# Performance work log

Measured on AMD Instinct MI355X. Metric: run time of the kernel, lower is better.

The kernel has to match this reference:

```python
import jax, jax.numpy as jnp
import numpy as np
import math

B, S, E = 2, 2048, 1024
H = 16
D = E // H  # head dim = 64


def setup_inputs() -> dict:
    key = jax.random.key(0)
    ks = jax.random.split(key, 9)
    s = 1.0 / math.sqrt(E)
    return {
        "x": jax.random.normal(ks[0], (B, S, E), dtype=jnp.float32),
        "Wq": jax.random.uniform(ks[1], (E, E), jnp.float32, -s, s),
        "bq": jnp.zeros((E,), jnp.float32),
        "Wk": jax.random.uniform(ks[2], (E, E), jnp.float32, -s, s),
        "bk": jnp.zeros((E,), jnp.float32),
        "Wv": jax.random.uniform(ks[3], (E, E), jnp.float32, -s, s),
        "bv": jnp.zeros((E,), jnp.float32),
        "Wo": jax.random.uniform(ks[4], (E, E), jnp.float32, -s, s),
        "bo": jnp.zeros((E,), jnp.float32),
    }


def reference(x, Wq, bq, Wk, bk, Wv, bv, Wo, bo):
    b, s, e = x.shape
    q = x @ Wq + bq  # [B,S,E]
    k = x @ Wk + bk
    v = x @ Wv + bv
    # [B,S,E] -> [B,H,S,D]
    q = q.reshape(b, s, H, D).transpose(0, 2, 1, 3)
    k = k.reshape(b, s, H, D).transpose(0, 2, 1, 3)
    v = v.reshape(b, s, H, D).transpose(0, 2, 1, 3)
    scores = jnp.einsum('bhqd,bhkd->bhqk', q, k) / jnp.sqrt(jnp.float32(D))
    causal = jnp.tril(jnp.ones((s, s), dtype=bool))  # keep lower triangle
    scores = jnp.where(causal, scores, -jnp.inf)
    attn = jax.nn.softmax(scores, axis=-1)
    # dropout is identity in eval mode
    out = jnp.einsum('bhqk,bhkd->bhqd', attn, v)
    out = out.transpose(0, 2, 1, 3).reshape(b, s, e)
    return out @ Wo + bo
```

## Files before the change

kernel.cpp:

```cpp
#include <hip/hip_runtime.h>
#include <hip/hip_bf16.h>
#include <math.h>

#define B_ 2
#define S_ 2048
#define E_ 1024
#define H_ 16
#define D_ 64
#define M_ (B_*S_)

typedef __attribute__((ext_vector_type(8))) short short8v;
typedef __attribute__((ext_vector_type(4))) float floatx4;

__device__ __forceinline__ short f2bf(float f) {
    union { float f; unsigned u; } x; x.f = f;
    unsigned r = (x.u + 0x7fffu + ((x.u >> 16) & 1u)) >> 16;
    return (short)r;
}

__device__ __forceinline__ unsigned pk_bf16(float a, float b) {
    union { float f; unsigned u; } x, y;
    x.f = a; y.f = b;
    return __builtin_amdgcn_perm(y.u + 0x8000u, x.u + 0x8000u, 0x07060302u);
}

__device__ __forceinline__ float fast_exp2(float x) {
#if __has_builtin(__builtin_amdgcn_exp2f)
    return __builtin_amdgcn_exp2f(x);
#else
    return __expf(x * 0.6931471805599453f);
#endif
}

__device__ __forceinline__ void gl2lds16(const void* g, void* l) {
    __builtin_amdgcn_global_load_lds(
        (const __attribute__((address_space(1))) void*)g,
        (__attribute__((address_space(3))) void*)l, 16, 0, 0);
}

__device__ __forceinline__ int swz_off(int row, int cg) {
    return row*64 + (((cg ^ (row & 7)) & 7) << 3);
}

__global__ __launch_bounds__(256) void prep(
    const float* __restrict__ x, short* __restrict__ xb,
    const float* __restrict__ W0, const float* __restrict__ W1,
    const float* __restrict__ W2, const float* __restrict__ W3,
    short* __restrict__ T0, short* __restrict__ T1,
    short* __restrict__ T2, short* __restrict__ T3)
{
    const int bid = blockIdx.x;
    if (bid < 2048) {
        const size_t i = ((size_t)bid*256 + threadIdx.x) * 8;
        float4 a = *(const float4*)(x + i);
        float4 b = *(const float4*)(x + i + 4);
        int4 p = { (int)pk_bf16(a.x,a.y), (int)pk_bf16(a.z,a.w),
                   (int)pk_bf16(b.x,b.y), (int)pk_bf16(b.z,b.w) };
        *(int4*)(xb + i) = p;
        return;
    }
    const int tb = bid - 2048;
    const int z = tb >> 10;
    const float* W = (z==0)?W0:(z==1)?W1:(z==2)?W2:W3;
    short*       T = (z==0)?T0:(z==1)?T1:(z==2)?T2:T3;
    __shared__ float tile[32][33];
    const int k0 = ((tb>>5)&31)*32, n0 = (tb&31)*32;
    const int r = threadIdx.x >> 5, c = threadIdx.x & 31;
    #pragma unroll
    for (int i=0;i<4;i++)
        tile[r+8*i][c] = W[(size_t)(k0+r+8*i)*E_ + n0 + c];
    __syncthreads();
    #pragma unroll
    for (int i=0;i<4;i++)
        T[(size_t)(n0+r+8*i)*E_ + k0 + c] = f2bf(tile[c][r+8*i]);
}

__global__ __launch_bounds__(512, 2) void qkv_gemm(
    const short* __restrict__ xb, const short* __restrict__ Wt,
    const float* __restrict__ bq, const float* __restrict__ bk, const float* __restrict__ bv,
    short* __restrict__ Qo, short* __restrict__ Ko, short* __restrict__ Vo)
{
    __shared__ __align__(16) short As[2][256*64];
    __shared__ __align__(16) short Bs[2][192*64];

    const int t = threadIdx.x;
    const int wave = t >> 6, lane = t & 63;
    const int quad = lane >> 4, l15 = lane & 15;
    const int wr = wave >> 2, wc = wave & 3;

    const int bid = blockIdx.x;
    const int sw  = (bid & 7) * 32 + (bid >> 3);
    const int m0  = (sw >> 4) * 256;
    const int nf0 = (sw & 15) * 192;

    const int sr8 = lane >> 3;
    const int scs = ((lane & 7) ^ sr8) * 8;

    const short* Ag = xb + (size_t)m0  * E_;
    const short* Bg = Wt + (size_t)nf0 * E_;

    floatx4 acc[8][3];
    #pragma unroll
    for (int i=0;i<8;i++)
        #pragma unroll
        for (int j=0;j<3;j++) acc[i][j] = (floatx4){0.f,0.f,0.f,0.f};

    auto stageA = [&](int p, int h, int kt) {
        const int rb = h*128 + wave*16;
        const short* src = Ag + (size_t)(rb + sr8)*E_ + kt*64 + scs;
        #pragma unroll
        for (int c=0;c<2;c++)
            gl2lds16(src + (size_t)c*8*E_, &As[p][(rb + c*8)*64]);
    };
    auto stageB = [&](int p, int u, int kt) {
        const int rb = u*64 + wave*8;
        gl2lds16(Bg + (size_t)(rb + sr8)*E_ + kt*64 + scs, &Bs[p][rb*64]);
    };

    short8v a[2][2], b[3][2];
    auto rdA = [&](int p, int row16, int ks) -> short8v {
        return *(const short8v*)&As[p][swz_off(wr*128 + row16*16 + l15, quad + ks*4)];
    };
    auto rdB = [&](int p, int row16, int ks) -> short8v {
        return *(const short8v*)&Bs[p][swz_off(wc*48 + row16*16 + l15, quad + ks*4)];
    };
    auto lda2 = [&](int p, int mbase) {
        #pragma unroll
        for (int j=0;j<2;j++)
            #pragma unroll
            for (int ks=0;ks<2;ks++) a[j][ks] = rdA(p, mbase+j, ks);
    };
    auto mm = [&](int mbase) {
        #pragma unroll
        for (int j=0;j<2;j++)
            #pragma unroll
            for (int nt=0;nt<3;nt++)
                #pragma unroll
                for (int ks=0;ks<2;ks++)
                    acc[mbase+j][nt] = __builtin_amdgcn_mfma_f32_16x16x32_bf16(
                        a[j][ks], b[nt][ks], acc[mbase+j][nt], 0,0,0);
    };

    auto ktile = [&](int tt, int p) {
        #pragma unroll
        for (int nt=0;nt<3;nt++)
            #pragma unroll
            for (int ks=0;ks<2;ks++) b[nt][ks] = rdB(p, nt, ks);
        lda2(p, 0);
        if (tt+1 < 16) stageA(p^1, 0, tt+1);
        __builtin_amdgcn_s_barrier();
        __builtin_amdgcn_s_setprio(1);
        mm(0);
        __builtin_amdgcn_s_setprio(0);
        __builtin_amdgcn_s_barrier();
        lda2(p, 2);
        if (tt+1 < 16) stageA(p^1, 1, tt+1);
        __builtin_amdgcn_s_barrier();
        __builtin_amdgcn_s_setprio(1);
        mm(2);
        __builtin_amdgcn_s_setprio(0);
        __builtin_amdgcn_s_barrier();
        lda2(p, 4);
        if (tt+2 < 16) { stageB(p, 0, tt+2); stageB(p, 1, tt+2); }
        __builtin_amdgcn_s_barrier();
        __builtin_amdgcn_s_setprio(1);
        mm(4);
        __builtin_amdgcn_s_setprio(0);
        __builtin_amdgcn_s_barrier();
        lda2(p, 6);
        if (tt+2 < 16) stageB(p, 2, tt+2);
        __builtin_amdgcn_s_barrier();
        __builtin_amdgcn_s_setprio(1);
        mm(6);
        __builtin_amdgcn_s_setprio(0);
        if (tt+2 < 16)      asm volatile("s_waitcnt vmcnt(3)" ::: "memory");
        else if (tt+1 < 16) asm volatile("s_waitcnt vmcnt(0)" ::: "memory");
        __builtin_amdgcn_s_barrier();
    };

    stageA(0,0,0); stageA(0,1,0);
    stageB(0,0,0); stageB(0,1,0); stageB(0,2,0);
    stageB(1,0,1); stageB(1,1,1); stageB(1,2,1);
    asm volatile("s_waitcnt vmcnt(3)" ::: "memory");
    __builtin_amdgcn_s_barrier();

    #pragma unroll 1
    for (int tb = 0; tb < 16; tb += 2) {
        ktile(tb,   0);
        ktile(tb+1, 1);
    }

    #pragma unroll
    for (int nt=0;nt<3;nt++) {
        const int nwg = nf0 + wc*48 + nt*16 + l15;
        const int zf  = nwg >> 10;
        const float* bbf = (zf==0) ? bq : (zf==1) ? bk : bv;
        short* outf      = (zf==0) ? Qo : (zf==1) ? Ko : Vo;
        const float scf  = (zf==0) ? 0.18033688011112042f : 1.0f;
        const int nl = nwg & 1023;
        const float bias = bbf[nl];
        const int h = nl >> 6, d = nl & 63;
        #pragma unroll
        for (int mt=0;mt<8;mt++) {
            #pragma unroll
            for (int r=0;r<4;r++) {
                const int m = m0 + wr*128 + mt*16 + quad*4 + r;
                const int b2 = m >> 11, s = m & (S_-1);
                const int bh = (b2<<4) + h;
                const float v = (acc[mt][nt][r] + bias) * scf;
                if (zf == 0) {
                    outf[((size_t)bh*S_ + s)*D_ + d] = f2bf(v);
                } else if (zf == 1) {
                    const int ts = s >> 6, kk = s & 63;
                    const int c = kk*8 + ((d>>3) ^ ((kk>>2)&7));
                    outf[((size_t)bh*32 + ts)*4096 + c*8 + (d&7)] = f2bf(v);
                } else {
                    const int ts = s >> 6, sk = s & 63;
                    const int c = d*8 + ((sk>>3) ^ (d&7));
                    outf[((size_t)bh*32 + ts)*4096 + c*8 + (sk&7)] = f2bf(v);
                }
            }
        }
    }
}

__global__ __launch_bounds__(256, 3) void attn_kernel(
    const short* __restrict__ Q, const short* __restrict__ K, const short* __restrict__ V,
    short* __restrict__ AO)
{
    const int bh = blockIdx.x;
    const int qb = (gridDim.y - 1 - blockIdx.y) * 128;
    const int t = threadIdx.x;
    const int wave = t >> 6, lane = t & 63;
    const int quad = lane >> 4, l15 = lane & 15;

    const short* Qp = Q + (size_t)bh * (S_*D_);
    const short* Kp = K + (size_t)bh * (S_*D_);
    const short* Vp = V + (size_t)bh * (S_*D_);

    __shared__ __align__(16) short KVs[2][8192];
    __shared__ __align__(16) short Psl[4][2][16*72];

    const int qA = qb + wave*16;
    const int qB = qb + 64 + wave*16;
    const short* qa = Qp + (size_t)(qA + l15)*D_ + quad*8;
    const short8v qA0 = *(const short8v*)qa, qA1 = *(const short8v*)(qa + 32);
    const short* qbp = Qp + (size_t)(qB + l15)*D_ + quad*8;
    const short8v qB0 = *(const short8v*)qbp, qB1 = *(const short8v*)(qbp + 32);

    const int qrbA = qA + quad*4;
    const int qrbB = qB + quad*4;

    floatx4 oA[4], oB[4];
    #pragma unroll
    for (int i=0;i<4;i++) { oA[i] = (floatx4){0,0,0,0}; oB[i] = (floatx4){0,0,0,0}; }
    float tsA[4] = {0,0,0,0}, tsB[4] = {0,0,0,0};

    const int L = (qb >> 6) + 2;
    const int swz = l15 & 7;

    auto stage = [&](int kt, int p) {
        const short* src = ((wave < 2) ? Kp : Vp) + (size_t)kt*4096 + (wave&1)*2048 + lane*8;
        short* dst = &KVs[p][((wave < 2) ? 0 : 4096) + (wave&1)*2048];
        #pragma unroll
        for (int c=0;c<4;c++)
            gl2lds16(src + c*512, dst + c*512);
    };
    auto qk2 = [&](const short* KL, floatx4 (&sA)[4], floatx4 (&sB)[4]) {
        __builtin_amdgcn_s_setprio(1);
        #pragma unroll
        for (int h=0; h<4; h++) {
            const int rowc = (4*l15 + h)*8;
            short8v b0 = *(const short8v*)(KL + (rowc + (quad       ^ swz))*8);
            short8v b1 = *(const short8v*)(KL + (rowc + ((4 + quad) ^ swz))*8);
            sA[h] = (floatx4){0.f,0.f,0.f,0.f};
            sA[h] = __builtin_amdgcn_mfma_f32_16x16x32_bf16(qA0, b0, sA[h], 0,0,0);
            sA[h] = __builtin_amdgcn_mfma_f32_16x16x32_bf16(qA1, b1, sA[h], 0,0,0);
            sB[h] = (floatx4){0.f,0.f,0.f,0.f};
            sB[h] = __builtin_amdgcn_mfma_f32_16x16x32_bf16(qB0, b0, sB[h], 0,0,0);
            sB[h] = __builtin_amdgcn_mfma_f32_16x16x32_bf16(qB1, b1, sB[h], 0,0,0);
        }
        __builtin_amdgcn_s_setprio(0);
    };
    auto soft_u = [&](floatx4 (&s)[4], float* ts, short* pw, int qrb, int k0, bool masked) {
        const int kk = k0 + 4*l15;
        #pragma unroll
        for (int r=0; r<4; r++) {
            float p[4];
            if (masked) {
                const int qr = qrb + r;
                #pragma unroll
                for (int h=0; h<4; h++) {
                    const float e = fast_exp2(s[h][r]);
                    p[h] = (kk + h > qr) ? 0.f : e;
                }
            } else {
                #pragma unroll
                for (int h=0; h<4; h++) p[h] = fast_exp2(s[h][r]);
            }
            ts[r] += (p[0] + p[1]) + (p[2] + p[3]);
            int2 pkv = { (int)pk_bf16(p[0], p[1]), (int)pk_bf16(p[2], p[3]) };
            *(int2*)(pw + (quad*4 + r)*72 + l15*4) = pkv;
        }
    };
    short8v vr[4][2];
    auto loadv = [&](const short* VL) {
        #pragma unroll
        for (int dt=0; dt<4; dt++) {
            const int rowc = (dt*16 + l15)*8;
            vr[dt][0] = *(const short8v*)(VL + (rowc + (quad       ^ swz))*8);
            vr[dt][1] = *(const short8v*)(VL + (rowc + ((4 + quad) ^ swz))*8);
        }
    };
    auto pv = [&](const short* pw, floatx4 (&o)[4]) {
        const short8v pf0 = *(const short8v*)(pw + l15*72 + quad*8);
        const short8v pf1 = *(const short8v*)(pw + l15*72 + 32 + quad*8);
        __builtin_amdgcn_s_setprio(1);
        #pragma unroll
        for (int dt=0; dt<4; dt++) {
            o[dt] = __builtin_amdgcn_mfma_f32_16x16x32_bf16(pf0, vr[dt][0], o[dt], 0,0,0);
            o[dt] = __builtin_amdgcn_mfma_f32_16x16x32_bf16(pf1, vr[dt][1], o[dt], 0,0,0);
        }
        __builtin_amdgcn_s_setprio(0);
    };

    stage(0, 0);
    __syncthreads();
    stage(1, 1);
    {
        floatx4 sA[4], sB[4];
        qk2(&KVs[0][0], sA, sB);
        loadv(&KVs[0][4096]);
        const bool mk = (L <= 2);
        soft_u(sA, tsA, &Psl[wave][0][0], qrbA, 0, mk);
        soft_u(sB, tsB, &Psl[wave][1][0], qrbB, 0, mk);
    }

    for (int kt = 1; kt < L; kt++) {
        const int p = kt & 1;
        __syncthreads();
        if (kt + 1 < L) stage(kt + 1, p ^ 1);
        floatx4 sA[4], sB[4];
        qk2(&KVs[p][0], sA, sB);
        pv(&Psl[wave][0][0], oA);
        pv(&Psl[wave][1][0], oB);
        loadv(&KVs[p][4096]);
        const int k0 = kt << 6;
        const bool mk = (kt >= L - 2);
        soft_u(sA, tsA, &Psl[wave][0][0], qrbA, k0, mk);
        soft_u(sB, tsB, &Psl[wave][1][0], qrbB, k0, mk);
    }

    pv(&Psl[wave][0][0], oA);
    pv(&Psl[wave][1][0], oB);

    float lA[4], lB[4];
    #pragma unroll
    for (int r=0; r<4; r++) {
        float a = tsA[r], b = tsB[r];
        #pragma unroll
        for (int off=1; off<16; off<<=1) {
            a += __shfl_xor(a, off);
            b += __shfl_xor(b, off);
        }
        lA[r] = a; lB[r] = b;
    }

    const int b = bh >> 4, h = bh & 15;
    #pragma unroll
    for (int dt=0; dt<4; dt++) {
        #pragma unroll
        for (int r=0; r<4; r++) {
            const int d = dt*16 + l15;
            const int sA_ = qA + quad*4 + r;
            const int sB_ = qB + quad*4 + r;
            AO[((size_t)(b*S_ + sA_)*H_ + h)*D_ + d] = f2bf(oA[dt][r] / lA[r]);
            AO[((size_t)(b*S_ + sB_)*H_ + h)*D_ + d] = f2bf(oB[dt][r] / lB[r]);
        }
    }
}

__global__ __launch_bounds__(256) void out_gemm(
    const short* __restrict__ A, const short* __restrict__ Wto,
    const float* __restrict__ bo, float* __restrict__ out)
{
    __shared__ __align__(16) short As[128*64];
    __shared__ __align__(16) short Bs[64*64];

    const int t = threadIdx.x;
    const int wave = t >> 6, lane = t & 63;
    const int quad = lane >> 4, l15 = lane & 15;
    const int lin = blockIdx.x;
    const int m0 = (lin & 31) * 128;
    const int n0 = (lin >> 5) * 64;
    const int sr8 = lane >> 3;
    const int scs = ((lane & 7) ^ sr8) * 8;

    floatx4 acc[2][4];
    #pragma unroll
    for (int i=0;i<2;i++)
        #pragma unroll
        for (int j=0;j<4;j++) acc[i][j] = (floatx4){0.f,0.f,0.f,0.f};

    for (int k0 = 0; k0 < E_; k0 += 64) {
        #pragma unroll
        for (int c=0;c<4;c++) {
            const int rb = wave*32 + c*8;
            gl2lds16(A + (size_t)(m0+rb+sr8)*E_ + k0 + scs, &As[rb*64]);
        }
        #pragma unroll
        for (int c=0;c<2;c++) {
            const int rb = wave*16 + c*8;
            gl2lds16(Wto + (size_t)(n0+rb+sr8)*E_ + k0 + scs, &Bs[rb*64]);
        }
        __syncthreads();
        #pragma unroll
        for (int ks=0; ks<2; ks++) {
            const int cg = quad + ks*4;
            short8v a[2], b[4];
            #pragma unroll
            for (int mt=0;mt<2;mt++) a[mt] = *(const short8v*)&As[swz_off(wave*32+mt*16+l15, cg)];
            #pragma unroll
            for (int nt=0;nt<4;nt++) b[nt] = *(const short8v*)&Bs[swz_off(nt*16+l15, cg)];
            #pragma unroll
            for (int mt=0;mt<2;mt++)
                #pragma unroll
                for (int nt=0;nt<4;nt++)
                    acc[mt][nt] = __builtin_amdgcn_mfma_f32_16x16x32_bf16(a[mt], b[nt], acc[mt][nt], 0,0,0);
        }
        __syncthreads();
    }

    #pragma unroll
    for (int nt=0;nt<4;nt++) {
        const int n = n0 + nt*16 + l15;
        const float bias = bo[n];
        #pragma unroll
        for (int mt=0;mt<2;mt++) {
            #pragma unroll
            for (int r=0;r<4;r++) {
                const int m = m0 + wave*32 + mt*16 + quad*4 + r;
                out[(size_t)m*E_ + n] = acc[mt][nt][r] + bias;
            }
        }
    }
}

extern "C" void kernel_launch(void* const* d_in, const int* in_sizes, int n_in,
                              void* d_out, int out_size, void* d_ws, size_t ws_size,
                              hipStream_t stream)
{
    const float* x  = (const float*)d_in[0];
    const float* Wq = (const float*)d_in[1];
    const float* bq = (const float*)d_in[2];
    const float* Wk = (const float*)d_in[3];
    const float* bk = (const float*)d_in[4];
    const float* Wv = (const float*)d_in[5];
    const float* bv = (const float*)d_in[6];
    const float* Wo = (const float*)d_in[7];
    const float* bo = (const float*)d_in[8];

    short* xb  = (short*)d_ws;
    short* Tq  = xb  + (size_t)M_ * E_;
    short* Tk  = Tq  + (size_t)E_ * E_;
    short* Tv  = Tk  + (size_t)E_ * E_;
    short* To  = Tv  + (size_t)E_ * E_;
    short* Qw  = To  + (size_t)E_ * E_;
    short* Kw  = Qw  + (size_t)M_ * E_;
    short* Vw  = Kw  + (size_t)M_ * E_;
    short* AOw = Vw  + (size_t)M_ * E_;

    dim3 blk(256);
    prep<<<dim3(2048 + 4096), blk, 0, stream>>>(x, xb, Wq, Wk, Wv, Wo, Tq, Tk, Tv, To);
    qkv_gemm<<<dim3(256), dim3(512), 0, stream>>>(xb, Tq, bq, bk, bv, Qw, Kw, Vw);
    attn_kernel<<<dim3(B_*H_, S_/128), blk, 0, stream>>>(Qw, Kw, Vw, AOw);
    out_gemm<<<dim3(512), blk, 0, stream>>>(AOw, To, bo, (float*)d_out);
}
```

Measured before the change: 191.2 us.

## Halve attention query tile to 64 rows per block, doubling grid size

```diff
diff --git a/kernel.cpp b/kernel.cpp
--- a/kernel.cpp
+++ b/kernel.cpp
@@ -229,7 +229,7 @@
     short* __restrict__ AO)
 {
     const int bh = blockIdx.x;
-    const int qb = (gridDim.y - 1 - blockIdx.y) * 128;
+    const int qb = (gridDim.y - 1 - blockIdx.y) * 64;
     const int t = threadIdx.x;
     const int wave = t >> 6, lane = t & 63;
     const int quad = lane >> 4, l15 = lane & 15;
@@ -239,24 +239,19 @@
     const short* Vp = V + (size_t)bh * (S_*D_);
 
     __shared__ __align__(16) short KVs[2][8192];
-    __shared__ __align__(16) short Psl[4][2][16*72];
+    __shared__ __align__(16) short Psl[4][16*72];
 
     const int qA = qb + wave*16;
-    const int qB = qb + 64 + wave*16;
     const short* qa = Qp + (size_t)(qA + l15)*D_ + quad*8;
     const short8v qA0 = *(const short8v*)qa, qA1 = *(const short8v*)(qa + 32);
-    const short* qbp = Qp + (size_t)(qB + l15)*D_ + quad*8;
-    const short8v qB0 = *(const short8v*)qbp, qB1 = *(const short8v*)(qbp + 32);
-
     const int qrbA = qA + quad*4;
-    const int qrbB = qB + quad*4;
-
-    floatx4 oA[4], oB[4];
-    #pragma unroll
-    for (int i=0;i<4;i++) { oA[i] = (floatx4){0,0,0,0}; oB[i] = (floatx4){0,0,0,0}; }
-    float tsA[4] = {0,0,0,0}, tsB[4] = {0,0,0,0};
-
-    const int L = (qb >> 6) + 2;
+
+    floatx4 oA[4];
+    #pragma unroll
+    for (int i=0;i<4;i++) oA[i] = (floatx4){0,0,0,0};
+    float tsA[4] = {0,0,0,0};
+
+    const int L = (qb >> 6) + 1;
     const int swz = l15 & 7;
 
     auto stage = [&](int kt, int p) {
@@ -266,7 +261,7 @@
         for (int c=0;c<4;c++)
             gl2lds16(src + c*512, dst + c*512);
     };
-    auto qk2 = [&](const short* KL, floatx4 (&sA)[4], floatx4 (&sB)[4]) {
+    auto qk1 = [&](const short* KL, floatx4 (&sA)[4]) {
         __builtin_amdgcn_s_setprio(1);
         #pragma unroll
         for (int h=0; h<4; h++) {
@@ -276,9 +271,6 @@
             sA[h] = (floatx4){0.f,0.f,0.f,0.f};
             sA[h] = __builtin_amdgcn_mfma_f32_16x16x32_bf16(qA0, b0, sA[h], 0,0,0);
             sA[h] = __builtin_amdgcn_mfma_f32_16x16x32_bf16(qA1, b1, sA[h], 0,0,0);
-            sB[h] = (floatx4){0.f,0.f,0.f,0.f};
-            sB[h] = __builtin_amdgcn_mfma_f32_16x16x32_bf16(qB0, b0, sB[h], 0,0,0);
-            sB[h] = __builtin_amdgcn_mfma_f32_16x16x32_bf16(qB1, b1, sB[h], 0,0,0);
         }
         __builtin_amdgcn_s_setprio(0);
     };
@@ -326,44 +318,34 @@
 
     stage(0, 0);
     __syncthreads();
-    stage(1, 1);
+    if (L > 1) stage(1, 1);
     {
-        floatx4 sA[4], sB[4];
-        qk2(&KVs[0][0], sA, sB);
+        floatx4 sA[4];
+        qk1(&KVs[0][0], sA);
         loadv(&KVs[0][4096]);
-        const bool mk = (L <= 2);
-        soft_u(sA, tsA, &Psl[wave][0][0], qrbA, 0, mk);
-        soft_u(sB, tsB, &Psl[wave][1][0], qrbB, 0, mk);
+        soft_u(sA, tsA, &Psl[wave][0], qrbA, 0, L == 1);
     }
 
     for (int kt = 1; kt < L; kt++) {
         const int p = kt & 1;
         __syncthreads();
         if (kt + 1 < L) stage(kt + 1, p ^ 1);
-        floatx4 sA[4], sB[4];
-        qk2(&KVs[p][0], sA, sB);
-        pv(&Psl[wave][0][0], oA);
-        pv(&Psl[wave][1][0], oB);
+        floatx4 sA[4];
+        qk1(&KVs[p][0], sA);
+        pv(&Psl[wave][0], oA);
         loadv(&KVs[p][4096]);
-        const int k0 = kt << 6;
-        const bool mk = (kt >= L - 2);
-        soft_u(sA, tsA, &Psl[wave][0][0], qrbA, k0, mk);
-        soft_u(sB, tsB, &Psl[wave][1][0], qrbB, k0, mk);
-    }
-
-    pv(&Psl[wave][0][0], oA);
-    pv(&Psl[wave][1][0], oB);
-
-    float lA[4], lB[4];
+        soft_u(sA, tsA, &Psl[wave][0], qrbA, kt << 6, kt == L - 1);
+    }
+
+    pv(&Psl[wave][0], oA);
+
+    float lA[4];
     #pragma unroll
     for (int r=0; r<4; r++) {
-        float a = tsA[r], b = tsB[r];
-        #pragma unroll
-        for (int off=1; off<16; off<<=1) {
-            a += __shfl_xor(a, off);
-            b += __shfl_xor(b, off);
-        }
-        lA[r] = a; lB[r] = b;
+        float a = tsA[r];
+        #pragma unroll
+        for (int off=1; off<16; off<<=1) a += __shfl_xor(a, off);
+        lA[r] = a;
     }
 
     const int b = bh >> 4, h = bh & 15;
@@ -373,9 +355,7 @@
         for (int r=0; r<4; r++) {
             const int d = dt*16 + l15;
             const int sA_ = qA + quad*4 + r;
-            const int sB_ = qB + quad*4 + r;
             AO[((size_t)(b*S_ + sA_)*H_ + h)*D_ + d] = f2bf(oA[dt][r] / lA[r]);
-            AO[((size_t)(b*S_ + sB_)*H_ + h)*D_ + d] = f2bf(oB[dt][r] / lB[r]);
         }
     }
 }
@@ -473,6 +453,6 @@
     dim3 blk(256);
     prep<<<dim3(2048 + 4096), blk, 0, stream>>>(x, xb, Wq, Wk, Wv, Wo, Tq, Tk, Tv, To);
     qkv_gemm<<<dim3(256), dim3(512), 0, stream>>>(xb, Tq, bq, bk, bv, Qw, Kw, Vw);
-    attn_kernel<<<dim3(B_*H_, S_/128), blk, 0, stream>>>(Qw, Kw, Vw, AOw);
+    attn_kernel<<<dim3(B_*H_, S_/64), blk, 0, stream>>>(Qw, Kw, Vw, AOw);
     out_gemm<<<dim3(512), blk, 0, stream>>>(AOw, To, bo, (float*)d_out);
 }
```

Result: faster. 177.2 us (median of 3 runs) (-7.3%).
